# Kernel tuning notes

Hardware: AMD Instinct MI355X
Metric: run time of the kernel (lower is better)

The kernel has to match this reference:

```python
import jax, jax.numpy as jnp
import numpy as np

B, S, H = 4, 2048, 1024
NH, HD = 16, 64  # num heads, head dim
NUM_TASKS = 8


def setup_inputs() -> dict:
    key = jax.random.key(0)
    ks = jax.random.split(key, 12)
    sc = 1.0 / np.sqrt(H)
    return {
        "hidden_states": jax.random.normal(ks[0], (B, S, H), dtype=jnp.float32),
        "attention_mask": jnp.zeros((B, 1, 1, S), dtype=jnp.float32),
        "Wq": jax.random.normal(ks[1], (H, H), dtype=jnp.float32) * sc,
        "bq": jnp.zeros((H,), dtype=jnp.float32),
        "Wk": jax.random.normal(ks[2], (H, H), dtype=jnp.float32) * sc,
        "bk": jnp.zeros((H,), dtype=jnp.float32),
        "Wv": jax.random.normal(ks[3], (H, H), dtype=jnp.float32) * sc,
        "bv": jnp.zeros((H,), dtype=jnp.float32),
        "q_emb": jax.random.normal(ks[4], (NUM_TASKS, H), dtype=jnp.float32) * 0.02,
        "k_emb": jax.random.normal(ks[5], (NUM_TASKS, H), dtype=jnp.float32) * 0.02,
        "v_emb": jax.random.normal(ks[6], (NUM_TASKS, H), dtype=jnp.float32) * 0.02,
        "index": 3,
    }


def _split_heads(x):
    # [B,S,H] -> [B,NH,S,HD]
    b, s, _ = x.shape
    return x.reshape(b, s, NH, HD).transpose(0, 2, 1, 3)


def reference(hidden_states, attention_mask, Wq, bq, Wk, bk, Wv, bv,
              q_emb, k_emb, v_emb, index):
    # projections + per-task additive bias (broadcast over batch and seq)
    q = hidden_states @ Wq + bq + q_emb[index][None, None, :]
    k = hidden_states @ Wk + bk + k_emb[index][None, None, :]
    v = hidden_states @ Wv + bv + v_emb[index][None, None, :]

    q = _split_heads(q)  # [B,NH,S,HD]
    k = _split_heads(k)
    v = _split_heads(v)

    scores = jnp.einsum("bhqd,bhkd->bhqk", q, k) / np.sqrt(HD)
    scores = scores + attention_mask  # additive mask broadcasts [B,1,1,S]
    probs = jax.nn.softmax(scores, axis=-1)  # dropout prob 0 -> identity

    ctx = jnp.einsum("bhqk,bhkd->bhqd", probs, v)
    ctx = ctx.transpose(0, 2, 1, 3).reshape(hidden_states.shape[0], -1, H)
    return ctx
```

## Files before the change

### kernel.cpp

```cpp
#include <hip/hip_runtime.h>
#include <hip/hip_bf16.h>
#include <stdint.h>

#define BB 4
#define SS 2048
#define HH 1024
#define NHH 16
#define HDD 64
#define M_TOT (BB*SS)

#define XB_OFF 0
#define WT_OFF (M_TOT*HH)
#define Q_OFF  (WT_OFF + 3*HH*HH)
#define K_OFF  (Q_OFF + BB*NHH*SS*HDD)
#define VT_OFF (K_OFF + BB*NHH*SS*HDD)

typedef short bf16x8 __attribute__((ext_vector_type(8)));
typedef float f32x4  __attribute__((ext_vector_type(4)));

__device__ inline unsigned short f2bf(float f){
  unsigned u = __float_as_uint(f);
  u += 0x7fffu + ((u >> 16) & 1u);
  return (unsigned short)(u >> 16);
}
__device__ inline unsigned pk2bf(float lo, float hi){
  float2 t; t.x = lo; t.y = hi;
  __hip_bfloat162 h = __float22bfloat162_rn(t);
  return *(unsigned*)&h;
}

__device__ __forceinline__ void ld_g2l_16(const unsigned short* g, unsigned short* l){
  __builtin_amdgcn_global_load_lds(
      (const __attribute__((address_space(1))) void*)g,
      (__attribute__((address_space(3))) void*)l, 16, 0, 0);
}

__global__ void convert_x(const float* __restrict__ hs, unsigned short* __restrict__ xb){
  const int i = blockIdx.x*blockDim.x + threadIdx.x;
  float4 v = ((const float4*)hs)[i];
  ushort4 o;
  o.x = f2bf(v.x); o.y = f2bf(v.y); o.z = f2bf(v.z); o.w = f2bf(v.w);
  ((ushort4*)xb)[i] = o;
}

__global__ void convert_wt(const float* __restrict__ wq, const float* __restrict__ wk,
                           const float* __restrict__ wv, unsigned short* __restrict__ wt){
  __shared__ unsigned short t[64][65];
  const int z = blockIdx.z;
  const float* W = (z==0) ? wq : ((z==1) ? wk : wv);
  unsigned short* WT = wt + z*HH*HH;
  const int kb = blockIdx.x*64, nb = blockIdx.y*64;
  const int tid = threadIdx.x;
  #pragma unroll
  for (int i = 0; i < 16; i++){
    const int idx = i*256 + tid;
    const int r = idx >> 6, c = idx & 63;
    t[r][c] = f2bf(W[(kb + r)*HH + nb + c]);
  }
  __syncthreads();
  #pragma unroll
  for (int i = 0; i < 16; i++){
    const int idx = i*256 + tid;
    const int n = idx >> 6, k = idx & 63;
    WT[(nb + n)*HH + kb + k] = t[k][n];
  }
}

__global__ __launch_bounds__(256) void qkv_gemm(
    const unsigned short* __restrict__ ws16, unsigned short* __restrict__ wsq,
    const float* __restrict__ bq, const float* __restrict__ bk, const float* __restrict__ bv,
    const float* __restrict__ qe, const float* __restrict__ ke, const float* __restrict__ ve,
    const int* __restrict__ idxp){
  __shared__ unsigned short al[128*32];
  __shared__ unsigned short bl[128*32];

  const unsigned short* Xb = ws16 + XB_OFF;
  const int z = blockIdx.z;
  const unsigned short* Wt = ws16 + WT_OFF + z*HH*HH;
  const float* bias = (z==0) ? bq : ((z==1) ? bk : bv);
  const float* emb  = (z==0) ? qe : ((z==1) ? ke : ve);

  const int tid  = threadIdx.x;
  const int wv   = tid >> 6;
  const int ln   = tid & 63;
  const int quad = ln >> 4;
  const int l15  = ln & 15;
  const int m0 = blockIdx.x * 128;
  const int n0 = blockIdx.y * 128;
  const int wm = wv & 1, wn = wv >> 1;

  const int sr0 = wv*32 + (ln >> 2);
  const int sr1 = sr0 + 16;
  const int sk  = (ln & 3)*8;
  const unsigned short* ga0 = &Xb[(size_t)(m0 + sr0)*HH + sk];
  const unsigned short* ga1 = &Xb[(size_t)(m0 + sr1)*HH + sk];
  const unsigned short* gb0 = &Wt[(size_t)(n0 + sr0)*HH + sk];
  const unsigned short* gb1 = &Wt[(size_t)(n0 + sr1)*HH + sk];
  unsigned short* alb0 = &al[wv*1024];
  unsigned short* alb1 = &al[wv*1024 + 512];
  unsigned short* blb0 = &bl[wv*1024];
  unsigned short* blb1 = &bl[wv*1024 + 512];

  f32x4 acc[4][4] = {};

  for (int k0 = 0; k0 < HH; k0 += 32){
    __syncthreads();
    ld_g2l_16(ga0 + k0, alb0);
    ld_g2l_16(ga1 + k0, alb1);
    ld_g2l_16(gb0 + k0, blb0);
    ld_g2l_16(gb1 + k0, blb1);
    __syncthreads();

    bf16x8 af[4], bf[4];
    #pragma unroll
    for (int i = 0; i < 4; i++){
      af[i] = *(const bf16x8*)&al[(wm*64 + i*16 + l15)*32 + quad*8];
      bf[i] = *(const bf16x8*)&bl[(wn*64 + i*16 + l15)*32 + quad*8];
    }
    #pragma unroll
    for (int mi = 0; mi < 4; mi++)
      #pragma unroll
      for (int ni = 0; ni < 4; ni++)
        acc[mi][ni] = __builtin_amdgcn_mfma_f32_16x16x32_bf16(af[mi], bf[ni], acc[mi][ni], 0, 0, 0);
  }

  const int index = idxp[0];
  const float oscale = (z==0) ? 0.18033688011112042f : 1.0f;
  #pragma unroll
  for (int ni = 0; ni < 4; ni++){
    const int n = n0 + wn*64 + ni*16 + l15;
    const float biasv = bias[n] + emb[index*HH + n];
    const int h = n >> 6, d = n & 63;
    #pragma unroll
    for (int mi = 0; mi < 4; mi++){
      #pragma unroll
      for (int r = 0; r < 4; r++){
        const int g  = m0 + wm*64 + mi*16 + quad*4 + r;
        const int b_ = g >> 11;
        const int s_ = g & (SS - 1);
        const int bh = b_*NHH + h;
        const unsigned short val = f2bf((acc[mi][ni][r] + biasv) * oscale);
        if (z == 2)      wsq[VT_OFF + (size_t)(bh*HDD + d)*SS + s_] = val;
        else if (z == 0) wsq[Q_OFF  + (size_t)(bh*SS + s_)*HDD + d] = val;
        else             wsq[K_OFF  + (size_t)(bh*SS + s_)*HDD + d] = val;
      }
    }
  }
}

#define ST_P 40
__global__ __launch_bounds__(256, 4) void attn_mfma(
    const unsigned short* __restrict__ ws16,
    const float* __restrict__ mask, float* __restrict__ out){
  __shared__ __align__(16) unsigned short kb[2][32*64];
  __shared__ __align__(16) unsigned short vb[2][64*32];
  __shared__ __align__(16) unsigned short pb[4][32*ST_P];

  const int tid  = threadIdx.x;
  const int wave = tid >> 6;
  const int lane = tid & 63;
  const int quad = lane >> 4;
  const int l15  = lane & 15;
  const int qb   = blockIdx.x & 15;
  const int bh   = blockIdx.x >> 4;
  const int b    = bh >> 4, h = bh & 15;
  const int q0   = qb*128 + wave*32;
  const float LOG2E = 1.4426950408889634f;

  const unsigned short* Qg = ws16 + Q_OFF  + (size_t)bh*SS*HDD;
  const unsigned short* Kg = ws16 + K_OFF  + (size_t)bh*SS*HDD;
  const unsigned short* Vg = ws16 + VT_OFF + (size_t)bh*HDD*SS;
  const float* maskB = mask + b*SS;

  bf16x8 aq[2][2];
  #pragma unroll
  for (int qg = 0; qg < 2; qg++)
    #pragma unroll
    for (int h2 = 0; h2 < 2; h2++)
      aq[qg][h2] = *(const bf16x8*)(Qg + (size_t)(q0 + qg*16 + l15)*HDD + h2*32 + quad*8);

  const int kr = tid >> 3, kp = tid & 7;
  const int vr = tid >> 2, vp = tid & 3;
  const unsigned short* kSrc = Kg + (size_t)kr*HDD + ((((kp*16) ^ ((kr&7)<<4)))>>1);
  const unsigned short* vSrc = Vg + (size_t)vr*SS + vp*8;
  unsigned short* kDst = &kb[0][0] + (tid>>6)*512;
  unsigned short* vDst = &vb[0][0] + (tid>>6)*512;
  unsigned short* pw   = &pb[wave][0];

  f32x4 O[4][2] = {};
  float lacc[2] = {0.f, 0.f};

  ld_g2l_16(kSrc, kDst);
  ld_g2l_16(vSrc, vDst);
  __syncthreads();

  #pragma unroll 2
  for (int ch = 0; ch < 64; ++ch){
    const int cur = ch & 1;
    const int ktb = ch*32;
    if (ch < 63){
      ld_g2l_16(kSrc + (size_t)(ktb + 32)*HDD, kDst + (cur^1)*2048);
      ld_g2l_16(vSrc + (ktb + 32),             vDst + (cur^1)*2048);
    }
    const unsigned short* kcur = &kb[cur][0];
    const unsigned short* vcur = &vb[cur][0];

    bf16x8 ka[2][2];
    #pragma unroll
    for (int fi = 0; fi < 2; fi++)
      #pragma unroll
      for (int h2 = 0; h2 < 2; h2++){
        const int colb = (h2*64 + quad*16) ^ ((l15 & 7) << 4);
        ka[fi][h2] = *(const bf16x8*)&kcur[(fi*16 + l15)*64 + (colb>>1)];
      }

    #pragma unroll
    for (int fi = 0; fi < 2; fi++){
      const float4 mr = *(const float4*)(maskB + ktb + fi*16 + quad*4);
      f32x4 mv; mv[0]=mr.x*LOG2E; mv[1]=mr.y*LOG2E; mv[2]=mr.z*LOG2E; mv[3]=mr.w*LOG2E;
      #pragma unroll
      for (int qg = 0; qg < 2; qg++){
        f32x4 st = mv;
        st = __builtin_amdgcn_mfma_f32_16x16x32_bf16(ka[fi][0], aq[qg][0], st, 0,0,0);
        st = __builtin_amdgcn_mfma_f32_16x16x32_bf16(ka[fi][1], aq[qg][1], st, 0,0,0);
        f32x4 p;
        #pragma unroll
        for (int r = 0; r < 4; r++) p[r] = exp2f(st[r]);
        lacc[qg] += (p[0] + p[1]) + (p[2] + p[3]);
        uint2 w; w.x = pk2bf(p[0], p[1]); w.y = pk2bf(p[2], p[3]);
        *(uint2*)&pw[(qg*16 + l15)*ST_P + fi*16 + quad*4] = w;
      }
    }

    bf16x8 va[4];
    #pragma unroll
    for (int dg = 0; dg < 4; dg++)
      va[dg] = *(const bf16x8*)&vcur[(dg*16 + l15)*32 + quad*8];

    #pragma unroll
    for (int qg = 0; qg < 2; qg++){
      bf16x8 bp = *(const bf16x8*)&pw[(qg*16 + l15)*ST_P + quad*8];
      #pragma unroll
      for (int dg = 0; dg < 4; dg++)
        O[dg][qg] = __builtin_amdgcn_mfma_f32_16x16x32_bf16(va[dg], bp, O[dg][qg], 0,0,0);
    }

    __syncthreads();
  }

  float inv[2];
  #pragma unroll
  for (int qg = 0; qg < 2; qg++){
    float lq = lacc[qg];
    lq += __shfl_xor(lq, 16);
    lq += __shfl_xor(lq, 32);
    inv[qg] = 1.0f / lq;
  }

  #pragma unroll
  for (int qg = 0; qg < 2; qg++){
    float* op = out + ((size_t)b*SS + q0 + qg*16 + l15)*HH + h*HDD + quad*4;
    #pragma unroll
    for (int dg = 0; dg < 4; dg++){
      f32x4 v = O[dg][qg];
      float4 o; o.x = v[0]*inv[qg]; o.y = v[1]*inv[qg]; o.z = v[2]*inv[qg]; o.w = v[3]*inv[qg];
      *(float4*)(op + dg*16) = o;
    }
  }
}

extern "C" void kernel_launch(void* const* d_in, const int* in_sizes, int n_in,
                              void* d_out, int out_size, void* d_ws, size_t ws_size,
                              hipStream_t stream){
  const float* hs   = (const float*)d_in[0];
  const float* mask = (const float*)d_in[1];
  const float* Wq   = (const float*)d_in[2];
  const float* bq   = (const float*)d_in[3];
  const float* Wk   = (const float*)d_in[4];
  const float* bk   = (const float*)d_in[5];
  const float* Wv   = (const float*)d_in[6];
  const float* bv   = (const float*)d_in[7];
  const float* qe   = (const float*)d_in[8];
  const float* ke   = (const float*)d_in[9];
  const float* ve   = (const float*)d_in[10];
  const int*   idx  = (const int*)d_in[11];
  unsigned short* ws16 = (unsigned short*)d_ws;
  float* out = (float*)d_out;

  convert_x<<<M_TOT*HH/4/256, 256, 0, stream>>>(hs, ws16 + XB_OFF);
  dim3 gt(HH/64, HH/64, 3);
  convert_wt<<<gt, 256, 0, stream>>>(Wq, Wk, Wv, ws16 + WT_OFF);

  dim3 g2(M_TOT/128, HH/128, 3);
  qkv_gemm<<<g2, 256, 0, stream>>>(ws16, ws16, bq, bk, bv, qe, ke, ve, idx);

  attn_mfma<<<BB*NHH*SS/128, 256, 0, stream>>>(ws16, mask, out);
}
```

Baseline: 321.0 us.

## Use 512-thread attention blocks with 16 queries per wave and LDS mask

Doubles the attention block to 8 waves, each owning 16 query rows instead of 32, so the same K/V tile in LDS is shared by more waves. K and V loading is split so half the threads load K and half load V. The mask is prescaled once into LDS, exp2f is replaced by the hardware exp2 builtin, and block IDs are remapped to change the order in which heads and query blocks are scheduled. Each wave now has less MFMA work between barriers and holds fewer accumulator registers, which trades per-wave instruction-level parallelism for more waves in flight and more LDS traffic per unit of work.

```diff
diff --git a/kernel.cpp b/kernel.cpp
--- a/kernel.cpp
+++ b/kernel.cpp
@@ -149,22 +149,25 @@
 }
 
 #define ST_P 40
-__global__ __launch_bounds__(256, 4) void attn_mfma(
+__global__ __launch_bounds__(512, 6) void attn_mfma(
     const unsigned short* __restrict__ ws16,
     const float* __restrict__ mask, float* __restrict__ out){
   __shared__ __align__(16) unsigned short kb[2][32*64];
   __shared__ __align__(16) unsigned short vb[2][64*32];
-  __shared__ __align__(16) unsigned short pb[4][32*ST_P];
+  __shared__ __align__(16) unsigned short pb[8][16*ST_P];
+  __shared__ __align__(16) float mlds[SS];
 
   const int tid  = threadIdx.x;
   const int wave = tid >> 6;
   const int lane = tid & 63;
   const int quad = lane >> 4;
   const int l15  = lane & 15;
-  const int qb   = blockIdx.x & 15;
-  const int bh   = blockIdx.x >> 4;
+
+  const int bid  = (blockIdx.x & 7)*128 + (blockIdx.x >> 3);
+  const int qb   = bid & 15;
+  const int bh   = bid >> 4;
   const int b    = bh >> 4, h = bh & 15;
-  const int q0   = qb*128 + wave*32;
+  const int q0   = qb*128 + wave*16;
   const float LOG2E = 1.4426950408889634f;
 
   const unsigned short* Qg = ws16 + Q_OFF  + (size_t)bh*SS*HDD;
@@ -172,26 +175,39 @@
   const unsigned short* Vg = ws16 + VT_OFF + (size_t)bh*HDD*SS;
   const float* maskB = mask + b*SS;
 
-  bf16x8 aq[2][2];
-  #pragma unroll
-  for (int qg = 0; qg < 2; qg++)
-    #pragma unroll
-    for (int h2 = 0; h2 < 2; h2++)
-      aq[qg][h2] = *(const bf16x8*)(Qg + (size_t)(q0 + qg*16 + l15)*HDD + h2*32 + quad*8);
-
-  const int kr = tid >> 3, kp = tid & 7;
-  const int vr = tid >> 2, vp = tid & 3;
-  const unsigned short* kSrc = Kg + (size_t)kr*HDD + ((((kp*16) ^ ((kr&7)<<4)))>>1);
-  const unsigned short* vSrc = Vg + (size_t)vr*SS + vp*8;
-  unsigned short* kDst = &kb[0][0] + (tid>>6)*512;
-  unsigned short* vDst = &vb[0][0] + (tid>>6)*512;
-  unsigned short* pw   = &pb[wave][0];
-
-  f32x4 O[4][2] = {};
-  float lacc[2] = {0.f, 0.f};
-
-  ld_g2l_16(kSrc, kDst);
-  ld_g2l_16(vSrc, vDst);
+  {
+    float4 m4 = ((const float4*)maskB)[tid];
+    m4.x*=LOG2E; m4.y*=LOG2E; m4.z*=LOG2E; m4.w*=LOG2E;
+    *(float4*)&mlds[tid*4] = m4;
+  }
+
+  bf16x8 aq[2];
+  #pragma unroll
+  for (int h2 = 0; h2 < 2; h2++)
+    aq[h2] = *(const bf16x8*)(Qg + (size_t)(q0 + l15)*HDD + h2*32 + quad*8);
+
+  const unsigned short* sSrc;
+  unsigned short* sDst;
+  int sAdv;
+  if (tid < 256){
+    const int kr = tid >> 3, kp = tid & 7;
+    sSrc = Kg + (size_t)kr*HDD + ((((kp*16) ^ ((kr&7)<<4)))>>1);
+    sDst = &kb[0][0] + tid*8;
+    sAdv = 32*HDD;
+  } else {
+    const int t = tid - 256;
+    const int vr = t >> 2, vp = t & 3;
+    sSrc = Vg + (size_t)vr*SS + vp*8;
+    sDst = &vb[0][0] + t*8;
+    sAdv = 32;
+  }
+  unsigned short* pw = &pb[wave][0];
+
+  f32x4 O[4] = {};
+  float lacc = 0.f;
+
+  ld_g2l_16(sSrc, sDst);
+  const unsigned short* sp = sSrc + sAdv;
   __syncthreads();
 
   #pragma unroll 2
@@ -199,8 +215,8 @@
     const int cur = ch & 1;
     const int ktb = ch*32;
     if (ch < 63){
-      ld_g2l_16(kSrc + (size_t)(ktb + 32)*HDD, kDst + (cur^1)*2048);
-      ld_g2l_16(vSrc + (ktb + 32),             vDst + (cur^1)*2048);
+      ld_g2l_16(sp, sDst + (cur^1)*2048);
+      sp += sAdv;
     }
     const unsigned short* kcur = &kb[cur][0];
     const unsigned short* vcur = &vb[cur][0];
@@ -216,20 +232,15 @@
 
     #pragma unroll
     for (int fi = 0; fi < 2; fi++){
-      const float4 mr = *(const float4*)(maskB + ktb + fi*16 + quad*4);
-      f32x4 mv; mv[0]=mr.x*LOG2E; mv[1]=mr.y*LOG2E; mv[2]=mr.z*LOG2E; mv[3]=mr.w*LOG2E;
-      #pragma unroll
-      for (int qg = 0; qg < 2; qg++){
-        f32x4 st = mv;
-        st = __builtin_amdgcn_mfma_f32_16x16x32_bf16(ka[fi][0], aq[qg][0], st, 0,0,0);
-        st = __builtin_amdgcn_mfma_f32_16x16x32_bf16(ka[fi][1], aq[qg][1], st, 0,0,0);
-        f32x4 p;
-        #pragma unroll
-        for (int r = 0; r < 4; r++) p[r] = exp2f(st[r]);
-        lacc[qg] += (p[0] + p[1]) + (p[2] + p[3]);
-        uint2 w; w.x = pk2bf(p[0], p[1]); w.y = pk2bf(p[2], p[3]);
-        *(uint2*)&pw[(qg*16 + l15)*ST_P + fi*16 + quad*4] = w;
-      }
+      f32x4 st = *(const f32x4*)&mlds[ktb + fi*16 + quad*4];
+      st = __builtin_amdgcn_mfma_f32_16x16x32_bf16(ka[fi][0], aq[0], st, 0,0,0);
+      st = __builtin_amdgcn_mfma_f32_16x16x32_bf16(ka[fi][1], aq[1], st, 0,0,0);
+      f32x4 p;
+      #pragma unroll
+      for (int r = 0; r < 4; r++) p[r] = __builtin_amdgcn_exp2f(st[r]);
+      lacc += (p[0] + p[1]) + (p[2] + p[3]);
+      uint2 w; w.x = pk2bf(p[0], p[1]); w.y = pk2bf(p[2], p[3]);
+      *(uint2*)&pw[l15*ST_P + fi*16 + quad*4] = w;
     }
 
     bf16x8 va[4];
@@ -237,35 +248,27 @@
     for (int dg = 0; dg < 4; dg++)
       va[dg] = *(const bf16x8*)&vcur[(dg*16 + l15)*32 + quad*8];
 
-    #pragma unroll
-    for (int qg = 0; qg < 2; qg++){
-      bf16x8 bp = *(const bf16x8*)&pw[(qg*16 + l15)*ST_P + quad*8];
+    {
+      bf16x8 bp = *(const bf16x8*)&pw[l15*ST_P + quad*8];
       #pragma unroll
       for (int dg = 0; dg < 4; dg++)
-        O[dg][qg] = __builtin_amdgcn_mfma_f32_16x16x32_bf16(va[dg], bp, O[dg][qg], 0,0,0);
+        O[dg] = __builtin_amdgcn_mfma_f32_16x16x32_bf16(va[dg], bp, O[dg], 0,0,0);
     }
 
     __syncthreads();
   }
 
-  float inv[2];
-  #pragma unroll
-  for (int qg = 0; qg < 2; qg++){
-    float lq = lacc[qg];
-    lq += __shfl_xor(lq, 16);
-    lq += __shfl_xor(lq, 32);
-    inv[qg] = 1.0f / lq;
-  }
-
-  #pragma unroll
-  for (int qg = 0; qg < 2; qg++){
-    float* op = out + ((size_t)b*SS + q0 + qg*16 + l15)*HH + h*HDD + quad*4;
-    #pragma unroll
-    for (int dg = 0; dg < 4; dg++){
-      f32x4 v = O[dg][qg];
-      float4 o; o.x = v[0]*inv[qg]; o.y = v[1]*inv[qg]; o.z = v[2]*inv[qg]; o.w = v[3]*inv[qg];
-      *(float4*)(op + dg*16) = o;
-    }
+  float lq = lacc;
+  lq += __shfl_xor(lq, 16);
+  lq += __shfl_xor(lq, 32);
+  const float inv = 1.0f / lq;
+
+  float* op = out + ((size_t)b*SS + q0 + l15)*HH + h*HDD + quad*4;
+  #pragma unroll
+  for (int dg = 0; dg < 4; dg++){
+    f32x4 v = O[dg];
+    float4 o; o.x = v[0]*inv; o.y = v[1]*inv; o.z = v[2]*inv; o.w = v[3]*inv;
+    *(float4*)(op + dg*16) = o;
   }
 }
 
@@ -294,5 +297,5 @@
   dim3 g2(M_TOT/128, HH/128, 3);
   qkv_gemm<<<g2, 256, 0, stream>>>(ws16, ws16, bq, bk, bv, qe, ke, ve, idx);
 
-  attn_mfma<<<BB*NHH*SS/128, 256, 0, stream>>>(ws16, mask, out);
-}
+  attn_mfma<<<BB*NHH*SS/128, 512, 0, stream>>>(ws16, mask, out);
+}
```

After: 292.6 us. 8.8% less time.
